# Optimization experiments

Hardware: AMD Instinct MI355X
Metric: run time of the kernel (lower is better)

## Reference

```python
import jax, jax.numpy as jnp
import numpy as np

B, N, D, S, H = 64, 4096, 256, 8, 512
ITERS = 3
EPS = 1e-8
SCALE = D ** -0.5
LN_EPS = 1e-5


def _ln(x, w, b):
    mu = jnp.mean(x, axis=-1, keepdims=True)
    var = jnp.var(x, axis=-1, keepdims=True)
    return (x - mu) * jax.lax.rsqrt(var + LN_EPS) * w + b


def setup_inputs() -> dict:
    key = jax.random.key(0)
    ks = jax.random.split(key, 20)
    g = lambda k, shape, s=0.02: jax.random.normal(k, shape, dtype=jnp.float32) * s
    return {
        "inputs": jax.random.normal(ks[0], (B, N, D), dtype=jnp.float32),
        "query_pos": jax.random.uniform(ks[1], (1, S, D), dtype=jnp.float32),
        "wq": g(ks[2], (D, D)), "bq": jnp.zeros((D,), jnp.float32),
        "wk": g(ks[3], (D, D)), "bk": jnp.zeros((D,), jnp.float32),
        "wv": g(ks[4], (D, D)), "bv": jnp.zeros((D,), jnp.float32),
        "w_ih": g(ks[5], (3 * D, D)), "b_ih": jnp.zeros((3 * D,), jnp.float32),
        "w_hh": g(ks[6], (3 * D, D)), "b_hh": jnp.zeros((3 * D,), jnp.float32),
        "w1": g(ks[7], (H, D)), "b1": jnp.zeros((H,), jnp.float32),
        "w2": g(ks[8], (D, H)), "b2": jnp.zeros((D,), jnp.float32),
        "ln_in_w": jnp.ones((D,), jnp.float32), "ln_in_b": jnp.zeros((D,), jnp.float32),
        "ln_s_w": jnp.ones((D,), jnp.float32), "ln_s_b": jnp.zeros((D,), jnp.float32),
        "ln_ff_w": jnp.ones((D,), jnp.float32), "ln_ff_b": jnp.zeros((D,), jnp.float32),
    }


def _step(slots, k, v, wq, bq, w_ih, b_ih, w_hh, b_hh, w1, b1, w2, b2,
          ln_s_w, ln_s_b, ln_ff_w, ln_ff_b):
    s = _ln(slots, ln_s_w, ln_s_b)
    q = s @ wq.T + bq                                  # [B,S,D]
    dots = jnp.einsum('bid,bjd->bij', q, k) * SCALE    # [B,S,N]
    attn = jax.nn.softmax(dots, axis=1) + EPS          # softmax over slots
    attn = attn / jnp.sum(attn, axis=-1, keepdims=True)
    updates = jnp.einsum('bjd,bij->bid', v, attn)      # [B,S,D]
    # GRUCell(input=updates, hidden=slots), PyTorch gate order r,z,n
    gx = updates @ w_ih.T + b_ih
    gh = slots @ w_hh.T + b_hh
    xr, xz, xn = jnp.split(gx, 3, axis=-1)
    hr, hz, hn = jnp.split(gh, 3, axis=-1)
    r = jax.nn.sigmoid(xr + hr)
    z = jax.nn.sigmoid(xz + hz)
    n = jnp.tanh(xn + r * hn)
    h = (1.0 - z) * n + z * slots
    ff = jnp.maximum(_ln(h, ln_ff_w, ln_ff_b) @ w1.T + b1, 0.0) @ w2.T + b2
    return h + ff


def reference(inputs, query_pos, wq, bq, wk, bk, wv, bv,
              w_ih, b_ih, w_hh, b_hh, w1, b1, w2, b2,
              ln_in_w, ln_in_b, ln_s_w, ln_s_b, ln_ff_w, ln_ff_b):
    b = inputs.shape[0]
    slots = jnp.broadcast_to(query_pos, (b, S, D))
    x = _ln(inputs, ln_in_w, ln_in_b)
    k = x @ wk.T + bk
    v = x @ wv.T + bv
    step = lambda s: _step(s, k, v, wq, bq, w_ih, b_ih, w_hh, b_hh,
                           w1, b1, w2, b2, ln_s_w, ln_s_b, ln_ff_w, ln_ff_b)
    for _ in range(ITERS):
        slots = step(slots)
    slots = step(jax.lax.stop_gradient(slots))
    return slots
```

## Files before the change

kernel.cpp:

```cpp
#include <hip/hip_runtime.h>
#include <hip/hip_bf16.h>

#define DEV __device__ __forceinline__
typedef unsigned short u16;
using s16x8  = __attribute__((ext_vector_type(8))) short;
using f32x4v = __attribute__((ext_vector_type(4))) float;

constexpr float SCALE  = 0.0625f;
constexpr float EPS    = 1e-8f;
constexpr float LN_EPS = 1e-5f;

DEV u16 f2bf(float f) {
    __hip_bfloat16 h = __float2bfloat16(f);
    u16 u; __builtin_memcpy(&u, &h, 2); return u;
}
DEV float bf2f(u16 u) {
    unsigned int x = ((unsigned int)u) << 16;
    float f; __builtin_memcpy(&f, &x, 4); return f;
}
DEV float ld1(const void* p, size_t i, int bf) {
    return bf ? bf2f(((const u16*)p)[i]) : ((const float*)p)[i];
}
DEV float warp_sum64(float v) {
    v += __shfl_xor(v, 1);  v += __shfl_xor(v, 2);  v += __shfl_xor(v, 4);
    v += __shfl_xor(v, 8);  v += __shfl_xor(v, 16); v += __shfl_xor(v, 32);
    return v;
}
DEV float sigf(float x) { return 1.f / (1.f + expf(-x)); }

DEV int ts_addr(int cb, int j) { return cb*632 + j*8 + ((j>>3)<<4); }

__global__ void k_sniff(const void* __restrict__ x, int* __restrict__ flag) {
    int lane = threadIdx.x;
    u16 u = ((const u16*)x)[lane * 2];
    float v = bf2f(u);
    bool bad = !(fabsf(v) <= 1024.0f);
    unsigned long long m = __ballot(bad);
    if (lane == 0) *flag = (m == 0ull) ? 1 : 0;
}

__global__ __launch_bounds__(256) void k_prep_misc(
    const void* bq, const void* bk, const void* bv, const void* bih, const void* bhh,
    const void* b1, const void* b2, const void* liw, const void* lib,
    const void* lsw, const void* lsb, const void* lfw, const void* lfb,
    float* o_bq, float* o_bk, float* o_bv, float* o_bih, float* o_bhh,
    float* o_b1, float* o_b2, float* o_liw, float* o_lib,
    float* o_lsw, float* o_lsb, float* o_lfw, float* o_lfb,
    const int* flagp) {
    int bf = *flagp;
    int i = blockIdx.x * 256 + threadIdx.x;
    if (i < 256) { o_bq[i]  = ld1(bq,  i, bf); return; } i -= 256;
    if (i < 256) { o_bk[i]  = ld1(bk,  i, bf); return; } i -= 256;
    if (i < 256) { o_bv[i]  = ld1(bv,  i, bf); return; } i -= 256;
    if (i < 768) { o_bih[i] = ld1(bih, i, bf); return; } i -= 768;
    if (i < 768) { o_bhh[i] = ld1(bhh, i, bf); return; } i -= 768;
    if (i < 512) { o_b1[i]  = ld1(b1,  i, bf); return; } i -= 512;
    if (i < 256) { o_b2[i]  = ld1(b2,  i, bf); return; } i -= 256;
    if (i < 256) { o_liw[i] = ld1(liw, i, bf); return; } i -= 256;
    if (i < 256) { o_lib[i] = ld1(lib, i, bf); return; } i -= 256;
    if (i < 256) { o_lsw[i] = ld1(lsw, i, bf); return; } i -= 256;
    if (i < 256) { o_lsb[i] = ld1(lsb, i, bf); return; } i -= 256;
    if (i < 256) { o_lfw[i] = ld1(lfw, i, bf); return; } i -= 256;
    if (i < 256) { o_lfb[i] = ld1(lfb, i, bf); }
}

__global__ __launch_bounds__(256) void k_prep_w(
    const void* wq, const void* wv, const void* wk,
    const void* wih, const void* whh, const void* w1, const void* w2,
    u16* wqT_b, u16* wvT_b, u16* wk2_b, u16* wih_b, u16* whh_b, u16* w1_b, u16* w2_b,
    const float* __restrict__ liw, const int* flagp) {
    int bf = *flagp;
    int i = blockIdx.x * 256 + threadIdx.x;
    if (i < 65536)  { int c=i>>8, d=i&255; wqT_b[i] = f2bf(ld1(wq, (size_t)d*256+c, bf)); return; } i -= 65536;
    if (i < 65536)  { int c=i>>8, d=i&255; wvT_b[i] = f2bf(ld1(wv, (size_t)d*256+c, bf)); return; } i -= 65536;
    if (i < 65536)  { int n=i>>8, d=i&255; wk2_b[i] = f2bf(ld1(wk, (size_t)d*256+n, bf) * liw[n]); return; } i -= 65536;
    if (i < 196608) { wih_b[i] = f2bf(ld1(wih, i, bf)); return; } i -= 196608;
    if (i < 196608) { whh_b[i] = f2bf(ld1(whh, i, bf)); return; } i -= 196608;
    if (i < 131072) { w1_b[i]  = f2bf(ld1(w1,  i, bf)); return; } i -= 131072;
    if (i < 131072) { w2_b[i]  = f2bf(ld1(w2,  i, bf)); }
}

__global__ __launch_bounds__(256) void k_prep_m(const void* __restrict__ wk,
    const float* __restrict__ liw, const float* __restrict__ lib,
    const float* __restrict__ bk_f, float* __restrict__ m1p, float* __restrict__ m2p,
    const int* flagp) {
    int bf = *flagp;
    int wave = threadIdx.x >> 6, lane = threadIdx.x & 63;
    int d = blockIdx.x * 4 + wave;
    float s1 = 0.f, s2 = 0.f;
#pragma unroll
    for (int t = 0; t < 4; t++) {
        int c = lane * 4 + t;
        float w = ld1(wk, (size_t)d * 256 + c, bf);
        s1 += w * lib[c];
        s2 += w * liw[c];
    }
    s1 = warp_sum64(s1); s2 = warp_sum64(s2);
    if (lane == 0) { m1p[d] = s1 + bk_f[d]; m2p[d] = -s2; }
}

__global__ __launch_bounds__(256) void k_prep_u(
    const void* __restrict__ wq, const void* __restrict__ wk, const void* __restrict__ wih,
    const float* __restrict__ m1p, const float* __restrict__ m2p,
    const float* __restrict__ bq_f, const float* __restrict__ bv_f,
    const float* __restrict__ liw,
    float* __restrict__ u1, float* __restrict__ u2, float* __restrict__ bq2,
    float* __restrict__ wibv, float* __restrict__ c12, const int* flagp) {
    int bf = *flagp;
    int wave = threadIdx.x >> 6, lane = threadIdx.x & 63;
    int idx = blockIdx.x * 4 + wave;
    if (idx >= 1538) return;
    float s = 0.f;
#pragma unroll
    for (int t = 0; t < 4; t++) {
        int d = lane * 4 + t;
        if (idx < 256)       s += ld1(wq, (size_t)d*256 + idx, bf) * m1p[d];
        else if (idx < 512)  s += ld1(wq, (size_t)d*256 + (idx-256), bf) * m2p[d];
        else if (idx < 768)  s += bq_f[d] * ld1(wk, (size_t)d*256 + (idx-512), bf);
        else if (idx < 1536) s += ld1(wih, (size_t)(idx-768)*256 + d, bf) * bv_f[d];
        else if (idx == 1536) s += bq_f[d] * m1p[d];
        else                  s += bq_f[d] * m2p[d];
    }
    s = warp_sum64(s);
    if (lane == 0) {
        if (idx < 256)       u1[idx] = s;
        else if (idx < 512)  u2[idx-256] = s;
        else if (idx < 768)  bq2[idx-512] = s * liw[idx-512];
        else if (idx < 1536) wibv[idx-768] = s;
        else                 c12[idx-1536] = s;
    }
}

__global__ __launch_bounds__(256) void k_stats(const void* __restrict__ x,
                                               u16* __restrict__ XB,
                                               float* __restrict__ mu,
                                               float* __restrict__ rs,
                                               const int* flagp) {
    int bf = *flagp;
    int wave = threadIdx.x >> 6, lane = threadIdx.x & 63;
    int row  = blockIdx.x * 4 + wave;
    float v[4];
    if (bf) {
        u16 a4[4];
        __builtin_memcpy(a4, (const u16*)x + (size_t)row * 256 + lane * 4, 8);
#pragma unroll
        for (int i = 0; i < 4; i++) v[i] = bf2f(a4[i]);
    } else {
        float4 f = *(const float4*)((const float*)x + (size_t)row * 256 + lane * 4);
        v[0]=f.x; v[1]=f.y; v[2]=f.z; v[3]=f.w;
        u16 b4[4];
#pragma unroll
        for (int i = 0; i < 4; i++) b4[i] = f2bf(v[i]);
        __builtin_memcpy(XB + (size_t)row * 256 + lane * 4, b4, 8);
    }
    float s  = v[0]+v[1]+v[2]+v[3];
    float s2 = v[0]*v[0]+v[1]*v[1]+v[2]*v[2]+v[3]*v[3];
    s = warp_sum64(s); s2 = warp_sum64(s2);
    if (lane == 0) {
        float m = s * (1.f/256.f);
        mu[row] = m;
        rs[row] = rsqrtf(s2 * (1.f/256.f) - m*m + LN_EPS);
    }
}

__global__ __launch_bounds__(256) void k_prep_s(const void* __restrict__ qp,
    const float* __restrict__ lsw, const float* __restrict__ lsb,
    const float* __restrict__ u1, const float* __restrict__ u2, const float* __restrict__ c12,
    float* __restrict__ slots, u16* __restrict__ Acat, u16* __restrict__ s_b,
    float* __restrict__ kap, float* __restrict__ lam, const int* flagp) {
    int bf = *flagp;
    int m = blockIdx.x;
    int s_ = m & 7, d = threadIdx.x;
    float v = ld1(qp, (size_t)s_ * 256 + d, bf);
    slots[(size_t)m*256 + d]   = v;
    Acat[(size_t)m*512 + 256 + d] = f2bf(v);
    __shared__ float red[16];
    float su = warp_sum64(v), sq = warp_sum64(v*v);
    int wave = threadIdx.x >> 6, lane = threadIdx.x & 63;
    if (lane == 0) { red[wave] = su; red[4+wave] = sq; }
    __syncthreads();
    float S1 = red[0]+red[1]+red[2]+red[3], S2 = red[4]+red[5]+red[6]+red[7];
    float muv = S1*(1.f/256.f);
    float rsv = rsqrtf(S2*(1.f/256.f) - muv*muv + LN_EPS);
    float sn = (v - muv)*rsv*lsw[d] + lsb[d];
    s_b[(size_t)m*256 + d] = f2bf(sn);
    float ks = warp_sum64(sn * u1[d]), ls = warp_sum64(sn * u2[d]);
    if (lane == 0) { red[8+wave] = ks; red[12+wave] = ls; }
    __syncthreads();
    if (threadIdx.x == 0) {
        kap[m] = red[8]+red[9]+red[10]+red[11] + c12[0];
        lam[m] = red[12]+red[13]+red[14]+red[15] + c12[1];
    }
}

template<bool OUT_BF16, bool RELU>
__global__ __launch_bounds__(256) void gemm64(
    const u16* __restrict__ A, const u16* __restrict__ W,
    const float* __restrict__ bias, void* __restrict__ outp, int Nn, int K) {
    int m0 = blockIdx.x * 64, n0 = blockIdx.y * 64;
    int tid = threadIdx.x;
    int wave = tid >> 6, lane = tid & 63, quad = lane >> 4, l15 = lane & 15;
    int wm = wave >> 1, wn = wave & 1;
    __shared__ __attribute__((aligned(16))) u16 A_s[64*40];
    __shared__ __attribute__((aligned(16))) u16 B_s[64*40];
    f32x4v acc[2][2];
#pragma unroll
    for (int i = 0; i < 2; i++)
#pragma unroll
        for (int j = 0; j < 2; j++) acc[i][j] = (f32x4v){0.f,0.f,0.f,0.f};
    int r0 = tid >> 2, seg = tid & 3;
    int nkc = K >> 5;
    for (int kc = 0; kc < nkc; ++kc) {
        s16x8 a0 = *(const s16x8*)(A + (size_t)(m0 + r0)*K + kc*32 + seg*8);
        s16x8 b0 = *(const s16x8*)(W + (size_t)(n0 + r0)*K + kc*32 + seg*8);
        __syncthreads();
        *(s16x8*)(A_s + r0*40 + seg*8) = a0;
        *(s16x8*)(B_s + r0*40 + seg*8) = b0;
        __syncthreads();
        s16x8 af[2], bfr[2];
#pragma unroll
        for (int t = 0; t < 2; t++) af[t]  = *(const s16x8*)(A_s + (wm*32 + t*16 + l15)*40 + quad*8);
#pragma unroll
        for (int t = 0; t < 2; t++) bfr[t] = *(const s16x8*)(B_s + (wn*32 + t*16 + l15)*40 + quad*8);
#pragma unroll
        for (int ti = 0; ti < 2; ti++)
#pragma unroll
            for (int tj = 0; tj < 2; tj++)
                acc[ti][tj] = __builtin_amdgcn_mfma_f32_16x16x32_bf16(af[ti], bfr[tj], acc[ti][tj], 0, 0, 0);
    }
#pragma unroll
    for (int tj = 0; tj < 2; tj++) {
        int colg = n0 + wn*32 + tj*16 + l15;
        float bv_ = bias ? bias[colg] : 0.f;
#pragma unroll
        for (int ti = 0; ti < 2; ti++) {
            int rowb = m0 + wm*32 + ti*16 + quad*4;
#pragma unroll
            for (int r = 0; r < 4; r++) {
                float v = acc[ti][tj][r] + bv_;
                if (RELU) v = fmaxf(v, 0.f);
                if (OUT_BF16) ((u16*)outp)[(size_t)(rowb + r)*Nn + colg] = f2bf(v);
                else          ((float*)outp)[(size_t)(rowb + r)*Nn + colg] = v;
            }
        }
    }
}

__global__ __launch_bounds__(256) void k_big(const u16* __restrict__ Wc2_b,
    const u16* __restrict__ whh_b, const float* __restrict__ bih_f,
    const float* __restrict__ bhh_f, const float* __restrict__ wibv,
    u16* __restrict__ Wbig, float* __restrict__ bbig) {
    int idx = blockIdx.x * 256 + threadIdx.x;
    int n = idx >> 9, k = idx & 511;
    u16 v;
    if (n < 512)      v = (k < 256) ? Wc2_b[(size_t)n*256 + k] : whh_b[(size_t)n*256 + (k-256)];
    else if (n < 768) v = (k < 256) ? Wc2_b[(size_t)n*256 + k] : (u16)0;
    else              v = (k < 256) ? (u16)0 : whh_b[(size_t)(n-256)*256 + (k-256)];
    Wbig[idx] = v;
    if (idx < 1024) {
        float bb;
        if (idx < 512)      bb = bih_f[idx] + wibv[idx] + bhh_f[idx];
        else if (idx < 768) bb = bih_f[idx] + wibv[idx];
        else                bb = bhh_f[idx-256];
        bbig[idx] = bb;
    }
}

__global__ __launch_bounds__(256) void k_attn(
    const void* __restrict__ xraw, const u16* __restrict__ XB,
    const u16* __restrict__ q2b,
    const float* __restrict__ kap, const float* __restrict__ lam,
    const float* __restrict__ mu, const float* __restrict__ rs,
    const int* __restrict__ flagp,
    float* __restrict__ Zp, float* __restrict__ Rp, float* __restrict__ Tp) {
    int bf = *flagp;
    const u16* xb = bf ? (const u16*)xraw : XB;
    int jcc = blockIdx.x;
    int b   = blockIdx.y;
    int tid = threadIdx.x;
    int wave = tid >> 6, lane = tid & 63, quad = lane >> 4, l15 = lane & 15;
    __shared__ __attribute__((aligned(16))) u16 q_s[8*264];
    __shared__ __attribute__((aligned(16))) u16 a_s[16*72];
    __shared__ __attribute__((aligned(16))) u16 T_s[32*632];
    __shared__ float kl_s[32];
    {
        int row = tid >> 5, seg = tid & 31;
        s16x8 qv = *(const s16x8*)(q2b + (size_t)(b*8 + row)*256 + seg*8);
        *(s16x8*)(q_s + row*264 + seg*8) = qv;
    }
    if (tid < 16) {
        kl_s[tid]      = (tid < 8) ? kap[b*8 + tid] : 0.f;
        kl_s[16 + tid] = (tid < 8) ? lam[b*8 + tid] : 0.f;
    }
    f32x4v accz[4];
#pragma unroll
    for (int t = 0; t < 4; t++) accz[t] = (f32x4v){0.f,0.f,0.f,0.f};
    float rtot[4] = {0.f,0.f,0.f,0.f}, ttot[4] = {0.f,0.f,0.f,0.f};
    int jb16 = wave * 16;
    int jrow = tid >> 5, cseg = tid & 31;

    for (int sub = 0; sub < 2; ++sub) {
        int jloc = (jcc*2 + sub) * 64;
        size_t jbase = (size_t)b*4096 + jloc;
        s16x8 sv[8];
#pragma unroll
        for (int it = 0; it < 8; ++it) {
            int j = it*8 + jrow;
            sv[it] = *(const s16x8*)(xb + (jbase + j)*256 + cseg*8);
        }
        size_t rowg = jbase + jb16 + l15;
        const u16* xbp = xb + rowg*256 + quad*8;
        s16x8 xv[8];
#pragma unroll
        for (int kc = 0; kc < 8; ++kc) xv[kc] = *(const s16x8*)(xbp + kc*32);
        __syncthreads();
#pragma unroll
        for (int it = 0; it < 8; ++it) {
            int j = it*8 + jrow;
            *(s16x8*)(T_s + ts_addr(cseg, j)) = sv[it];
        }
        f32x4v accd = (f32x4v){0.f,0.f,0.f,0.f};
#pragma unroll
        for (int kc = 0; kc < 8; ++kc) {
            s16x8 af;
            if (l15 < 8) af = *(const s16x8*)(q_s + l15*264 + kc*32 + quad*8);
            else         af = (s16x8){0,0,0,0,0,0,0,0};
            accd = __builtin_amdgcn_mfma_f32_16x16x32_bf16(af, xv[kc], accd, 0, 0, 0);
        }
        float rsj = rs[rowg], mrj = mu[rowg] * rsj;
        float dv[4];
#pragma unroll
        for (int r = 0; r < 4; r++)
            dv[r] = SCALE*(rsj*accd[r] + mrj*kl_s[16 + quad*4 + r] + kl_s[quad*4 + r]);
        float mx = fmaxf(fmaxf(dv[0], dv[1]), fmaxf(dv[2], dv[3]));
        mx = fmaxf(mx, __shfl_xor(mx, 16));
        float ev[4];
        float sum = 0.f;
#pragma unroll
        for (int r = 0; r < 4; r++) { ev[r] = expf(dv[r] - mx); sum += ev[r]; }
        sum += __shfl_xor(sum, 16);
        float inv = 1.f / sum;
#pragma unroll
        for (int r = 0; r < 4; r++) {
            float a = ev[r]*inv + EPS;
            rtot[r] += a;
            ttot[r] += a * mrj;
            a_s[(quad*4 + r)*72 + jb16 + l15] = f2bf(a * rsj);
        }
        __syncthreads();
#pragma unroll
        for (int ct = 0; ct < 4; ++ct) {
            int c = wave*64 + ct*16 + l15;
            int cb = c >> 3, e = c & 7;
#pragma unroll
            for (int kc2 = 0; kc2 < 2; ++kc2) {
                s16x8 af2 = *(const s16x8*)(a_s + l15*72 + kc2*32 + quad*8);
                s16x8 bv;
#pragma unroll
                for (int t = 0; t < 8; t++) {
                    int jj = kc2*32 + quad*8 + t;
                    bv[t] = (short)T_s[ts_addr(cb, jj) + e];
                }
                accz[ct] = __builtin_amdgcn_mfma_f32_16x16x32_bf16(af2, bv, accz[ct], 0, 0, 0);
            }
        }
    }
    if (quad < 2) {
#pragma unroll
        for (int ct = 0; ct < 4; ++ct) {
            int c = wave*64 + ct*16 + l15;
#pragma unroll
            for (int r = 0; r < 4; r++)
                Zp[((size_t)(b*32 + jcc)*8 + quad*4 + r)*256 + c] = accz[ct][r];
        }
    }
#pragma unroll
    for (int r = 0; r < 4; r++) {
        rtot[r] += __shfl_xor(rtot[r], 1);
        rtot[r] += __shfl_xor(rtot[r], 2);
        rtot[r] += __shfl_xor(rtot[r], 4);
        rtot[r] += __shfl_xor(rtot[r], 8);
        ttot[r] += __shfl_xor(ttot[r], 1);
        ttot[r] += __shfl_xor(ttot[r], 2);
        ttot[r] += __shfl_xor(ttot[r], 4);
        ttot[r] += __shfl_xor(ttot[r], 8);
    }
    if (l15 == 0 && quad < 2) {
        int base = ((b*32 + jcc)*4 + wave)*8 + quad*4;
#pragma unroll
        for (int r = 0; r < 4; r++) { Rp[base + r] = rtot[r]; Tp[base + r] = ttot[r]; }
    }
}

__global__ __launch_bounds__(256) void k_reduce(const float* __restrict__ Zp,
    const float* __restrict__ Rp, const float* __restrict__ Tp,
    const float* __restrict__ liw, const float* __restrict__ lib,
    u16* __restrict__ Acat) {
    int m = blockIdx.x;
    int b = m >> 3, i = m & 7, d = threadIdx.x;
    float z = 0.f;
#pragma unroll
    for (int c = 0; c < 32; c++) z += Zp[((size_t)(b*32 + c)*8 + i)*256 + d];
    float rv = 0.f, tv = 0.f;
    if (d < 128) {
        rv = Rp[(size_t)(b*128 + d)*8 + i];
        tv = Tp[(size_t)(b*128 + d)*8 + i];
    }
    __shared__ float redR[4], redT[4];
    rv = warp_sum64(rv); tv = warp_sum64(tv);
    int wave = d >> 6, lane = d & 63;
    if (lane == 0) { redR[wave] = rv; redT[wave] = tv; }
    __syncthreads();
    float R = redR[0]+redR[1]+redR[2]+redR[3];
    float T = redT[0]+redT[1]+redT[2]+redT[3];
    float ys = (liw[d]*(z - T) + lib[d]*R) / R;
    Acat[(size_t)m*512 + d] = f2bf(ys);
}

__global__ __launch_bounds__(256) void k_gates(const float* __restrict__ g,
    const float* __restrict__ slots, const float* __restrict__ lfw,
    const float* __restrict__ lfb, float* __restrict__ h, u16* __restrict__ hln_b) {
    int m = blockIdx.x, d = threadIdx.x;
    const float* gm = g + (size_t)m*1024;
    float r = sigf(gm[d]);
    float z = sigf(gm[256 + d]);
    float nn = tanhf(gm[512 + d] + r * gm[768 + d]);
    float hv = (1.f - z)*nn + z*slots[(size_t)m*256 + d];
    h[(size_t)m*256 + d] = hv;
    __shared__ float red[8];
    float su = warp_sum64(hv), sq = warp_sum64(hv*hv);
    int wave = threadIdx.x >> 6, lane = threadIdx.x & 63;
    if (lane == 0) { red[wave] = su; red[4+wave] = sq; }
    __syncthreads();
    float S1 = red[0]+red[1]+red[2]+red[3], S2 = red[4]+red[5]+red[6]+red[7];
    float muv = S1*(1.f/256.f);
    float rsv = rsqrtf(S2*(1.f/256.f) - muv*muv + LN_EPS);
    hln_b[(size_t)m*256 + d] = f2bf((hv - muv)*rsv*lfw[d] + lfb[d]);
}

__global__ __launch_bounds__(256) void k_residual(const float* __restrict__ h,
    const float* __restrict__ ff2, const float* __restrict__ lsw,
    const float* __restrict__ lsb, const float* __restrict__ u1,
    const float* __restrict__ u2, const float* __restrict__ c12,
    float* __restrict__ slots, u16* __restrict__ Acat, u16* __restrict__ s_b,
    float* __restrict__ kap, float* __restrict__ lam) {
    int m = blockIdx.x, d = threadIdx.x;
    float sv = h[(size_t)m*256 + d] + ff2[(size_t)m*256 + d];
    slots[(size_t)m*256 + d] = sv;
    Acat[(size_t)m*512 + 256 + d] = f2bf(sv);
    __shared__ float red[16];
    float su = warp_sum64(sv), sq = warp_sum64(sv*sv);
    int wave = threadIdx.x >> 6, lane = threadIdx.x & 63;
    if (lane == 0) { red[wave] = su; red[4+wave] = sq; }
    __syncthreads();
    float S1 = red[0]+red[1]+red[2]+red[3], S2 = red[4]+red[5]+red[6]+red[7];
    float muv = S1*(1.f/256.f);
    float rsv = rsqrtf(S2*(1.f/256.f) - muv*muv + LN_EPS);
    float sn = (sv - muv)*rsv*lsw[d] + lsb[d];
    s_b[(size_t)m*256 + d] = f2bf(sn);
    float ks = warp_sum64(sn * u1[d]), ls = warp_sum64(sn * u2[d]);
    if (lane == 0) { red[8+wave] = ks; red[12+wave] = ls; }
    __syncthreads();
    if (threadIdx.x == 0) {
        kap[m] = red[8]+red[9]+red[10]+red[11] + c12[0];
        lam[m] = red[12]+red[13]+red[14]+red[15] + c12[1];
    }
}

__global__ __launch_bounds__(256) void k_out(const float* __restrict__ slots,
                                             void* __restrict__ out, const int* flagp) {
    int bf = *flagp;
    int i = blockIdx.x * 256 + threadIdx.x;
    if (bf) ((u16*)out)[i] = f2bf(slots[i]);
    else    ((float*)out)[i] = slots[i];
}

extern "C" void kernel_launch(void* const* d_in, const int* in_sizes, int n_in,
                              void* d_out, int out_size, void* d_ws, size_t ws_size,
                              hipStream_t stream) {
    (void)in_sizes; (void)n_in; (void)out_size; (void)ws_size;
    const void* inputs    = d_in[0];
    const void* query_pos = d_in[1];
    const void* wq   = d_in[2];  const void* bq   = d_in[3];
    const void* wk   = d_in[4];  const void* bk   = d_in[5];
    const void* wv   = d_in[6];  const void* bv   = d_in[7];
    const void* w_ih = d_in[8];  const void* b_ih = d_in[9];
    const void* w_hh = d_in[10]; const void* b_hh = d_in[11];
    const void* w1   = d_in[12]; const void* b1   = d_in[13];
    const void* w2   = d_in[14]; const void* b2   = d_in[15];
    const void* ln_in_w = d_in[16]; const void* ln_in_b = d_in[17];
    const void* ln_s_w  = d_in[18]; const void* ln_s_b  = d_in[19];
    const void* ln_ff_w = d_in[20]; const void* ln_ff_b = d_in[21];

    char* w = (char*)d_ws;
    size_t off = 0;
    auto alloc = [&](size_t bytes) -> void* {
        void* p = w + off;
        off = (off + bytes + 255) & ~(size_t)255;
        return p;
    };
    u16*   XB     = (u16*)alloc(134217728);
    float* Zp     = (float*)alloc(16777216);
    float* gates  = (float*)alloc(2097152);
    u16*   Wbig_b = (u16*)alloc(1048576);
    u16*   Wc2_b  = (u16*)alloc(393216);
    u16*   Wc_b   = (u16*)alloc(131072);
    u16*   wqT_b  = (u16*)alloc(131072);
    u16*   wvT_b  = (u16*)alloc(131072);
    u16*   wk2_b  = (u16*)alloc(131072);
    u16*   wih_b  = (u16*)alloc(393216);
    u16*   whh_b  = (u16*)alloc(393216);
    u16*   w1_b   = (u16*)alloc(262144);
    u16*   w2_b   = (u16*)alloc(262144);
    float* mu     = (float*)alloc(1048576);
    float* rs     = (float*)alloc(1048576);
    float* slots  = (float*)alloc(524288);
    u16*   s_b    = (u16*)alloc(262144);
    u16*   Acat   = (u16*)alloc(524288);
    u16*   q2_b   = (u16*)alloc(262144);
    float* h      = (float*)alloc(524288);
    u16*   hln_b  = (u16*)alloc(262144);
    u16*   ff1_b  = (u16*)alloc(524288);
    float* ff2    = (float*)alloc(524288);
    float* Rp     = (float*)alloc(262144);
    float* Tp     = (float*)alloc(262144);
    float* bq_f   = (float*)alloc(1024);
    float* bk_f   = (float*)alloc(1024);
    float* bv_f   = (float*)alloc(1024);
    float* bih_f  = (float*)alloc(3072);
    float* bhh_f  = (float*)alloc(3072);
    float* b1_f   = (float*)alloc(2048);
    float* b2_f   = (float*)alloc(1024);
    float* liw_f  = (float*)alloc(1024);
    float* lib_f  = (float*)alloc(1024);
    float* lsw_f  = (float*)alloc(1024);
    float* lsb_f  = (float*)alloc(1024);
    float* lfw_f  = (float*)alloc(1024);
    float* lfb_f  = (float*)alloc(1024);
    float* m1p    = (float*)alloc(1024);
    float* m2p    = (float*)alloc(1024);
    float* u1     = (float*)alloc(1024);
    float* u2     = (float*)alloc(1024);
    float* bq2    = (float*)alloc(1024);
    float* wibv   = (float*)alloc(3072);
    float* bbig   = (float*)alloc(4096);
    float* c12    = (float*)alloc(256);
    float* kap    = (float*)alloc(2048);
    float* lam    = (float*)alloc(2048);
    int*   flag   = (int*)alloc(256);

    k_sniff<<<1, 64, 0, stream>>>(inputs, flag);
    k_prep_misc<<<18, 256, 0, stream>>>(bq, bk, bv, b_ih, b_hh, b1, b2,
                                        ln_in_w, ln_in_b, ln_s_w, ln_s_b, ln_ff_w, ln_ff_b,
                                        bq_f, bk_f, bv_f, bih_f, bhh_f, b1_f, b2_f,
                                        liw_f, lib_f, lsw_f, lsb_f, lfw_f, lfb_f, flag);
    k_stats<<<65536, 256, 0, stream>>>(inputs, XB, mu, rs, flag);
    k_prep_w<<<3328, 256, 0, stream>>>(wq, wv, wk, w_ih, w_hh, w1, w2,
                                       wqT_b, wvT_b, wk2_b, wih_b, whh_b, w1_b, w2_b,
                                       liw_f, flag);
    k_prep_m<<<64, 256, 0, stream>>>(wk, liw_f, lib_f, bk_f, m1p, m2p, flag);
    k_prep_u<<<385, 256, 0, stream>>>(wq, wk, w_ih, m1p, m2p, bq_f, bv_f, liw_f,
                                      u1, u2, bq2, wibv, c12, flag);
    k_prep_s<<<512, 256, 0, stream>>>(query_pos, lsw_f, lsb_f, u1, u2, c12,
                                      slots, Acat, s_b, kap, lam, flag);
    gemm64<true, false><<<dim3(4, 4), 256, 0, stream>>>(wk2_b, wqT_b, nullptr, Wc_b, 256, 256);
    gemm64<true, false><<<dim3(12, 4), 256, 0, stream>>>(wih_b, wvT_b, nullptr, Wc2_b, 256, 256);
    k_big<<<2048, 256, 0, stream>>>(Wc2_b, whh_b, bih_f, bhh_f, wibv, Wbig_b, bbig);

    for (int step = 0; step < 4; ++step) {
        gemm64<true, false><<<dim3(8, 4), 256, 0, stream>>>(s_b, Wc_b, bq2, q2_b, 256, 256);
        k_attn<<<dim3(32, 64), 256, 0, stream>>>(inputs, XB, q2_b, kap, lam, mu, rs, flag, Zp, Rp, Tp);
        k_reduce<<<512, 256, 0, stream>>>(Zp, Rp, Tp, liw_f, lib_f, Acat);
        gemm64<false, false><<<dim3(8, 16), 256, 0, stream>>>(Acat, Wbig_b, bbig, gates, 1024, 512);
        k_gates<<<512, 256, 0, stream>>>(gates, slots, lfw_f, lfb_f, h, hln_b);
        gemm64<true, true ><<<dim3(8, 8), 256, 0, stream>>>(hln_b, w1_b, b1_f, ff1_b, 512, 256);
        gemm64<false, false><<<dim3(8, 4), 256, 0, stream>>>(ff1_b, w2_b, b2_f, ff2, 256, 512);
        k_residual<<<512, 256, 0, stream>>>(h, ff2, lsw_f, lsb_f, u1, u2, c12,
                                            slots, Acat, s_b, kap, lam);
    }
    k_out<<<512, 256, 0, stream>>>(slots, d_out, flag);
}
```

Before: 726.1 us.

## Fuse query projection into slot-LN kernels and reuse fragment loads for transpose

Removes the per-step q-projection GEMM launch by computing q2 = LN(slots)·Wc + bq2 inside k_prep_s and k_residual. It uses an fp32 Wc matrix and a shared-memory copy of the normalized slots, so the bf16 s_b buffer goes away. The prep kernel is moved after the Wc GEMM because it now depends on Wc. Separately, k_attn now fills its transposed shared tile from the MFMA operand registers it already loaded, instead of doing a second global load of the same x tile. The fused matvec reads 256 KB of fp32 weights per block with scalar-style FMAs, which trades one launch for slower per-block work.

After: 766.4 us. 5.6% more time.

```diff
diff --git a/kernel.cpp b/kernel.cpp
--- a/kernel.cpp
+++ b/kernel.cpp
@@ -166,8 +166,10 @@
 __global__ __launch_bounds__(256) void k_prep_s(const void* __restrict__ qp,
     const float* __restrict__ lsw, const float* __restrict__ lsb,
     const float* __restrict__ u1, const float* __restrict__ u2, const float* __restrict__ c12,
-    float* __restrict__ slots, u16* __restrict__ Acat, u16* __restrict__ s_b,
-    float* __restrict__ kap, float* __restrict__ lam, const int* flagp) {
+    const float* __restrict__ WcF, const float* __restrict__ bq2,
+    float* __restrict__ slots, u16* __restrict__ Acat,
+    float* __restrict__ kap, float* __restrict__ lam,
+    u16* __restrict__ q2b, const int* flagp) {
     int bf = *flagp;
     int m = blockIdx.x;
     int s_ = m & 7, d = threadIdx.x;
@@ -175,6 +177,7 @@
     slots[(size_t)m*256 + d]   = v;
     Acat[(size_t)m*512 + 256 + d] = f2bf(v);
     __shared__ float red[16];
+    __shared__ float sn_s[256];
     float su = warp_sum64(v), sq = warp_sum64(v*v);
     int wave = threadIdx.x >> 6, lane = threadIdx.x & 63;
     if (lane == 0) { red[wave] = su; red[4+wave] = sq; }
@@ -183,7 +186,7 @@
     float muv = S1*(1.f/256.f);
     float rsv = rsqrtf(S2*(1.f/256.f) - muv*muv + LN_EPS);
     float sn = (v - muv)*rsv*lsw[d] + lsb[d];
-    s_b[(size_t)m*256 + d] = f2bf(sn);
+    sn_s[d] = sn;
     float ks = warp_sum64(sn * u1[d]), ls = warp_sum64(sn * u2[d]);
     if (lane == 0) { red[8+wave] = ks; red[12+wave] = ls; }
     __syncthreads();
@@ -191,6 +194,15 @@
         kap[m] = red[8]+red[9]+red[10]+red[11] + c12[0];
         lam[m] = red[12]+red[13]+red[14]+red[15] + c12[1];
     }
+    float acc = 0.f;
+    const float4* wrow = (const float4*)(WcF + (size_t)d * 256);
+#pragma unroll 8
+    for (int kk = 0; kk < 64; ++kk) {
+        float4 wv = wrow[kk];
+        acc += sn_s[kk*4+0]*wv.x + sn_s[kk*4+1]*wv.y
+             + sn_s[kk*4+2]*wv.z + sn_s[kk*4+3]*wv.w;
+    }
+    q2b[(size_t)m*256 + d] = f2bf(acc + bq2[d]);
 }
 
 template<bool OUT_BF16, bool RELU>
@@ -297,17 +309,10 @@
     for (int t = 0; t < 4; t++) accz[t] = (f32x4v){0.f,0.f,0.f,0.f};
     float rtot[4] = {0.f,0.f,0.f,0.f}, ttot[4] = {0.f,0.f,0.f,0.f};
     int jb16 = wave * 16;
-    int jrow = tid >> 5, cseg = tid & 31;
 
     for (int sub = 0; sub < 2; ++sub) {
         int jloc = (jcc*2 + sub) * 64;
         size_t jbase = (size_t)b*4096 + jloc;
-        s16x8 sv[8];
-#pragma unroll
-        for (int it = 0; it < 8; ++it) {
-            int j = it*8 + jrow;
-            sv[it] = *(const s16x8*)(xb + (jbase + j)*256 + cseg*8);
-        }
         size_t rowg = jbase + jb16 + l15;
         const u16* xbp = xb + rowg*256 + quad*8;
         s16x8 xv[8];
@@ -315,10 +320,8 @@
         for (int kc = 0; kc < 8; ++kc) xv[kc] = *(const s16x8*)(xbp + kc*32);
         __syncthreads();
 #pragma unroll
-        for (int it = 0; it < 8; ++it) {
-            int j = it*8 + jrow;
-            *(s16x8*)(T_s + ts_addr(cseg, j)) = sv[it];
-        }
+        for (int kc = 0; kc < 8; ++kc)
+            *(s16x8*)(T_s + ts_addr(kc*4 + quad, jb16 + l15)) = xv[kc];
         f32x4v accd = (f32x4v){0.f,0.f,0.f,0.f};
 #pragma unroll
         for (int kc = 0; kc < 8; ++kc) {
@@ -442,13 +445,16 @@
     const float* __restrict__ ff2, const float* __restrict__ lsw,
     const float* __restrict__ lsb, const float* __restrict__ u1,
     const float* __restrict__ u2, const float* __restrict__ c12,
-    float* __restrict__ slots, u16* __restrict__ Acat, u16* __restrict__ s_b,
-    float* __restrict__ kap, float* __restrict__ lam) {
+    const float* __restrict__ WcF, const float* __restrict__ bq2,
+    float* __restrict__ slots, u16* __restrict__ Acat,
+    float* __restrict__ kap, float* __restrict__ lam,
+    u16* __restrict__ q2b) {
     int m = blockIdx.x, d = threadIdx.x;
     float sv = h[(size_t)m*256 + d] + ff2[(size_t)m*256 + d];
     slots[(size_t)m*256 + d] = sv;
     Acat[(size_t)m*512 + 256 + d] = f2bf(sv);
     __shared__ float red[16];
+    __shared__ float sn_s[256];
     float su = warp_sum64(sv), sq = warp_sum64(sv*sv);
     int wave = threadIdx.x >> 6, lane = threadIdx.x & 63;
     if (lane == 0) { red[wave] = su; red[4+wave] = sq; }
@@ -457,7 +463,7 @@
     float muv = S1*(1.f/256.f);
     float rsv = rsqrtf(S2*(1.f/256.f) - muv*muv + LN_EPS);
     float sn = (sv - muv)*rsv*lsw[d] + lsb[d];
-    s_b[(size_t)m*256 + d] = f2bf(sn);
+    sn_s[d] = sn;
     float ks = warp_sum64(sn * u1[d]), ls = warp_sum64(sn * u2[d]);
     if (lane == 0) { red[8+wave] = ks; red[12+wave] = ls; }
     __syncthreads();
@@ -465,6 +471,15 @@
         kap[m] = red[8]+red[9]+red[10]+red[11] + c12[0];
         lam[m] = red[12]+red[13]+red[14]+red[15] + c12[1];
     }
+    float acc = 0.f;
+    const float4* wrow = (const float4*)(WcF + (size_t)d * 256);
+#pragma unroll 8
+    for (int kk = 0; kk < 64; ++kk) {
+        float4 wv = wrow[kk];
+        acc += sn_s[kk*4+0]*wv.x + sn_s[kk*4+1]*wv.y
+             + sn_s[kk*4+2]*wv.z + sn_s[kk*4+3]*wv.w;
+    }
+    q2b[(size_t)m*256 + d] = f2bf(acc + bq2[d]);
 }
 
 __global__ __launch_bounds__(256) void k_out(const float* __restrict__ slots,
@@ -504,7 +519,7 @@
     float* gates  = (float*)alloc(2097152);
     u16*   Wbig_b = (u16*)alloc(1048576);
     u16*   Wc2_b  = (u16*)alloc(393216);
-    u16*   Wc_b   = (u16*)alloc(131072);
+    float* WcF    = (float*)alloc(262144);
     u16*   wqT_b  = (u16*)alloc(131072);
     u16*   wvT_b  = (u16*)alloc(131072);
     u16*   wk2_b  = (u16*)alloc(131072);
@@ -515,7 +530,6 @@
     float* mu     = (float*)alloc(1048576);
     float* rs     = (float*)alloc(1048576);
     float* slots  = (float*)alloc(524288);
-    u16*   s_b    = (u16*)alloc(262144);
     u16*   Acat   = (u16*)alloc(524288);
     u16*   q2_b   = (u16*)alloc(262144);
     float* h      = (float*)alloc(524288);
@@ -561,14 +575,13 @@
     k_prep_m<<<64, 256, 0, stream>>>(wk, liw_f, lib_f, bk_f, m1p, m2p, flag);
     k_prep_u<<<385, 256, 0, stream>>>(wq, wk, w_ih, m1p, m2p, bq_f, bv_f, liw_f,
                                       u1, u2, bq2, wibv, c12, flag);
-    k_prep_s<<<512, 256, 0, stream>>>(query_pos, lsw_f, lsb_f, u1, u2, c12,
-                                      slots, Acat, s_b, kap, lam, flag);
-    gemm64<true, false><<<dim3(4, 4), 256, 0, stream>>>(wk2_b, wqT_b, nullptr, Wc_b, 256, 256);
+    gemm64<false, false><<<dim3(4, 4), 256, 0, stream>>>(wk2_b, wqT_b, nullptr, WcF, 256, 256);
     gemm64<true, false><<<dim3(12, 4), 256, 0, stream>>>(wih_b, wvT_b, nullptr, Wc2_b, 256, 256);
     k_big<<<2048, 256, 0, stream>>>(Wc2_b, whh_b, bih_f, bhh_f, wibv, Wbig_b, bbig);
+    k_prep_s<<<512, 256, 0, stream>>>(query_pos, lsw_f, lsb_f, u1, u2, c12,
+                                      WcF, bq2, slots, Acat, kap, lam, q2_b, flag);
 
     for (int step = 0; step < 4; ++step) {
-        gemm64<true, false><<<dim3(8, 4), 256, 0, stream>>>(s_b, Wc_b, bq2, q2_b, 256, 256);
         k_attn<<<dim3(32, 64), 256, 0, stream>>>(inputs, XB, q2_b, kap, lam, mu, rs, flag, Zp, Rp, Tp);
         k_reduce<<<512, 256, 0, stream>>>(Zp, Rp, Tp, liw_f, lib_f, Acat);
         gemm64<false, false><<<dim3(8, 16), 256, 0, stream>>>(Acat, Wbig_b, bbig, gates, 1024, 512);
@@ -576,7 +589,7 @@
         gemm64<true, true ><<<dim3(8, 8), 256, 0, stream>>>(hln_b, w1_b, b1_f, ff1_b, 512, 256);
         gemm64<false, false><<<dim3(8, 4), 256, 0, stream>>>(ff1_b, w2_b, b2_f, ff2, 256, 512);
         k_residual<<<512, 256, 0, stream>>>(h, ff2, lsw_f, lsb_f, u1, u2, c12,
-                                            slots, Acat, s_b, kap, lam);
+                                            WcF, bq2, slots, Acat, kap, lam, q2_b);
     }
     k_out<<<512, 256, 0, stream>>>(slots, d_out, flag);
 }
```
